# Optimization experiments

Measured on AMD Instinct MI355X. Metric: run time of the kernel, lower is better.

## Reference

```python
import jax, jax.numpy as jnp
import numpy as np

H = 384
W = 384
C_X = 64       # channels of x (== out_channels)
C_PTX = 64     # channels of ptx
C_IN = C_X + C_PTX  # Linear in_channels = 128
C_OUT = 64
N_TGT = 120000  # number of target pixels (CSR segments)
DEG = 8         # points per target pixel
N_PTS = N_TGT * DEG


def setup_inputs() -> dict:
    key = jax.random.key(0)
    k1, k2, k3, k4 = jax.random.split(key, 4)
    x = jax.random.normal(k1, (1, C_X, H, W), jnp.float32)
    ptx = jax.random.normal(k2, (N_PTS, C_PTX), jnp.float32)
    # CSR row pointer over points per target pixel (monotone, ends at N_PTS)
    point_key = jnp.arange(N_TGT + 1, dtype=jnp.int32) * DEG
    # unique target-pixel indices into H*W
    pixel_tgt_idx = jnp.arange(N_TGT, dtype=jnp.int32)
    sm_w = jax.random.normal(k3, (C_IN, 1), jnp.float32) * 0.05
    sm_b = jnp.zeros((1,), jnp.float32)
    fo_w = jax.random.normal(k4, (C_IN, C_OUT), jnp.float32) * 0.05
    fo_b = jnp.zeros((C_OUT,), jnp.float32)
    return {"x": x, "ptx": ptx, "sm_w": sm_w, "sm_b": sm_b,
            "fo_w": fo_w, "fo_b": fo_b, "point_key": point_key,
            "pixel_tgt_idx": pixel_tgt_idx, "bs": 1, "height": H, "width": W}


def reference(x, ptx, sm_w, sm_b, fo_w, fo_b, point_key, pixel_tgt_idx, bs, height, width):
    # segment id per point from CSR rowptr (static total length for jit)
    seg = jnp.repeat(jnp.arange(N_TGT, dtype=jnp.int32), jnp.diff(point_key),
                     total_repeat_length=N_PTS)
    # pixel features gathered to target pixels, then CSR-gathered to points
    feat_px = x.transpose(0, 2, 3, 1).reshape(height * width, C_X)[pixel_tgt_idx]
    feat = jnp.concatenate([ptx, feat_px[seg]], axis=1)  # [N_PTS, C_IN]
    # _net_forward: identity (base class)
    # segment softmax over points within each pixel group
    logits = feat @ sm_w + sm_b  # [N_PTS, 1]
    m = jax.ops.segment_max(logits, seg, num_segments=N_TGT)
    e = jnp.exp(logits - m[seg])
    s = jax.ops.segment_sum(e, seg, num_segments=N_TGT)
    weight = e / (s[seg] + 1e-16)
    # feat_out projection replaces ptx
    ptx_out = feat @ fo_w + fo_b  # [N_PTS, C_OUT]
    agg = jax.ops.segment_sum(weight * ptx_out, seg, num_segments=N_TGT)  # [N_TGT, C_OUT]
    # list_to_map: scatter aggregated features back to image grid + mask
    flat = jnp.zeros((height * width, C_OUT), x.dtype).at[pixel_tgt_idx].set(agg)
    mask = jnp.zeros((height * width, 1), x.dtype).at[pixel_tgt_idx].set(1.0)
    fmap = flat.reshape(1, height, width, C_OUT).transpose(0, 3, 1, 2)
    mmap = mask.reshape(1, height, width, 1).transpose(0, 3, 1, 2)
    x_out = jnp.where(mmap > 0, fmap, x)
    return x_out, ptx_out
```

## Files before the change

kernel.cpp:

```cpp
#include <hip/hip_runtime.h>
#include <hip/hip_bf16.h>
#include <math.h>

typedef __attribute__((ext_vector_type(8))) short short8v;
typedef __attribute__((ext_vector_type(4))) float float4v;

__device__ __forceinline__ short f2bf(float f) {
    __hip_bfloat16 h = __float2bfloat16(f);
    short s;
    __builtin_memcpy(&s, &h, sizeof(short));
    return s;
}

__device__ __forceinline__ float4v mfma_bf16(short8v a, short8v b, float4v c) {
    return __builtin_amdgcn_mfma_f32_16x16x32_bf16(a, b, c, 0, 0, 0);
}

__global__ __launch_bounds__(256)
void copy_x_kernel(const float4* __restrict__ x, float4* __restrict__ out, int n4) {
    int i = blockIdx.x * blockDim.x + threadIdx.x;
    if (i < n4) out[i] = x[i];
}

__global__ __launch_bounds__(256, 3)
void fused_kernel(const float* __restrict__ x,
                  const float* __restrict__ ptx,
                  const float* __restrict__ sm_w,
                  const float* __restrict__ fo_w,
                  const float* __restrict__ fo_b,
                  const int* __restrict__ point_key,
                  const int* __restrict__ pixel_tgt_idx,
                  float* __restrict__ xout,
                  float* __restrict__ ptx_out,
                  int n_tgt, int n_pts, int hw)
{
    __shared__ unsigned short fpx[32][72];
    __shared__ float q_lds[32][68];
    __shared__ float agg_lds[32][68];
    __shared__ int pix_s[32], r0_s[32], deg_s[32];

    const int tid  = threadIdx.x;
    const int lane = tid & 63;
    const int w    = tid >> 6;
    const int t0   = blockIdx.x * 32;
    const int lo16 = lane & 15;
    const int g    = lane >> 4;

    if (tid < 32) {
        int t = t0 + tid;
        bool v = t < n_tgt;
        int r0 = v ? point_key[t] : 0;
        int d  = v ? (point_key[t + 1] - r0) : 0;
        pix_s[tid] = v ? pixel_tgt_idx[t] : 0;
        r0_s[tid]  = r0;
        deg_s[tid] = d > 8 ? 8 : d;
    }
    __syncthreads();

    {
        int tgt = tid & 31, cq = tid >> 5;
        int pix = pix_s[tgt];
        #pragma unroll
        for (int i = 0; i < 8; ++i) {
            int c = cq * 8 + i;
            fpx[tgt][c] = (unsigned short)f2bf(x[(size_t)c * hw + pix]);
        }
    }
    __syncthreads();

    {
        const int mt_q = w & 1;
        const int ctb  = (w >> 1) * 2;
        short8v b2[2][2];
        #pragma unroll
        for (int ci = 0; ci < 2; ++ci)
            #pragma unroll
            for (int kh = 0; kh < 2; ++kh) {
                short8v bb;
                int col = (ctb + ci) * 16 + lo16;
                int kbase = kh * 32 + g * 8;
                #pragma unroll
                for (int j = 0; j < 8; ++j)
                    bb[j] = f2bf(fo_w[(size_t)(64 + kbase + j) * 64 + col]);
                b2[ci][kh] = bb;
            }
        short8v a2[2];
        #pragma unroll
        for (int kh = 0; kh < 2; ++kh) {
            int row = mt_q * 16 + lo16;
            a2[kh] = *(const short8v*)&fpx[row][kh * 32 + g * 8];
        }
        float4v qc0 = {0.f, 0.f, 0.f, 0.f}, qc1 = {0.f, 0.f, 0.f, 0.f};
        qc0 = mfma_bf16(a2[0], b2[0][0], qc0);
        qc0 = mfma_bf16(a2[1], b2[0][1], qc0);
        qc1 = mfma_bf16(a2[0], b2[1][0], qc1);
        qc1 = mfma_bf16(a2[1], b2[1][1], qc1);
        #pragma unroll
        for (int ci = 0; ci < 2; ++ci) {
            int col = (ctb + ci) * 16 + lo16;
            float fb = fo_b[col];
            const float4v& qc = ci ? qc1 : qc0;
            #pragma unroll
            for (int r = 0; r < 4; ++r)
                q_lds[mt_q * 16 + g * 4 + r][col] = qc[r] + fb;
        }
    }

    short8v b1[5][2];
    #pragma unroll
    for (int ct = 0; ct < 5; ++ct)
        #pragma unroll
        for (int kh = 0; kh < 2; ++kh) {
            short8v bb;
            int kbase = kh * 32 + g * 8;
            #pragma unroll
            for (int j = 0; j < 8; ++j) {
                int k = kbase + j;
                float f = (ct < 4) ? fo_w[(size_t)k * 64 + ct * 16 + lo16]
                                   : ((lo16 == 0) ? sm_w[k] : 0.0f);
                bb[j] = f2bf(f);
            }
            b1[ct][kh] = bb;
        }
    __syncthreads();

    const int tw0 = w * 8;
    #pragma unroll
    for (int mt = 0; mt < 4; ++mt) {
        int s_row = mt * 16 + lo16;
        int tlA   = tw0 + (s_row >> 3);
        int pg    = r0_s[tlA] + (s_row & 7);
        if (pg >= n_pts) pg = n_pts - 1;
        const float* prow = ptx + (size_t)pg * 64 + g * 8;
        short8v a[2];
        #pragma unroll
        for (int kh = 0; kh < 2; ++kh) {
            float4 f0 = *(const float4*)(prow + kh * 32);
            float4 f1 = *(const float4*)(prow + kh * 32 + 4);
            short8v aa;
            aa[0] = f2bf(f0.x); aa[1] = f2bf(f0.y); aa[2] = f2bf(f0.z); aa[3] = f2bf(f0.w);
            aa[4] = f2bf(f1.x); aa[5] = f2bf(f1.y); aa[6] = f2bf(f1.z); aa[7] = f2bf(f1.w);
            a[kh] = aa;
        }
        float4v c[5];
        #pragma unroll
        for (int ct = 0; ct < 5; ++ct) {
            float4v z = {0.f, 0.f, 0.f, 0.f};
            z = mfma_bf16(a[0], b1[ct][0], z);
            c[ct] = mfma_bf16(a[1], b1[ct][1], z);
        }

        const int tE   = tw0 + mt * 2 + (g >> 1);
        const int degE = deg_s[tE];
        const int r0E  = r0_s[tE];
        float lgt[4];
        #pragma unroll
        for (int r = 0; r < 4; ++r) {
            float v = __shfl(c[4][r], lane & 48);
            lgt[r] = (((g & 1) * 4 + r) < degE) ? v : -3.4e38f;
        }
        float m4 = fmaxf(fmaxf(lgt[0], lgt[1]), fmaxf(lgt[2], lgt[3]));
        float m8 = fmaxf(m4, __shfl_xor(m4, 16));
        float wgt[4], wsum = 0.f;
        #pragma unroll
        for (int r = 0; r < 4; ++r) {
            int pE = (g & 1) * 4 + r;
            wgt[r] = (pE < degE) ? __expf(lgt[r] - m8) : 0.0f;
            wsum += wgt[r];
        }
        wsum += __shfl_xor(wsum, 16);
        float inv = 1.0f / (wsum + 1e-16f);

        #pragma unroll
        for (int ct = 0; ct < 4; ++ct) {
            int col = ct * 16 + lo16;
            float qv = q_lds[tE][col];
            float ap = 0.f;
            #pragma unroll
            for (int r = 0; r < 4; ++r) {
                float po = c[ct][r] + qv;
                int pE = (g & 1) * 4 + r;
                if (pE < degE)
                    ptx_out[(size_t)(r0E + pE) * 64 + col] = po;
                ap = fmaf(wgt[r] * inv, po, ap);
            }
            ap += __shfl_xor(ap, 16);
            if (!(lane & 16))
                agg_lds[tE][col] = ap;
        }
    }
    __syncthreads();

    {
        int tgt = tid & 31, cq = tid >> 5;
        if (t0 + tgt < n_tgt) {
            int pix = pix_s[tgt];
            #pragma unroll
            for (int i = 0; i < 8; ++i) {
                int c = cq * 8 + i;
                xout[(size_t)c * hw + pix] = agg_lds[tgt][c];
            }
        }
    }
}

extern "C" void kernel_launch(void* const* d_in, const int* in_sizes, int n_in,
                              void* d_out, int out_size, void* d_ws, size_t ws_size,
                              hipStream_t stream) {
    const float* x             = (const float*)d_in[0];
    const float* ptx           = (const float*)d_in[1];
    const float* sm_w          = (const float*)d_in[2];
    const float* fo_w          = (const float*)d_in[4];
    const float* fo_b          = (const float*)d_in[5];
    const int*   point_key     = (const int*)d_in[6];
    const int*   pixel_tgt_idx = (const int*)d_in[7];

    const int x_elems = in_sizes[0];
    const int hw      = x_elems / 64;
    const int n_tgt   = in_sizes[7];
    const int n_pts   = in_sizes[1] / 64;

    float* xout    = (float*)d_out;
    float* ptx_out = xout + (size_t)x_elems;

    const int n4 = x_elems / 4;
    copy_x_kernel<<<(n4 + 255) / 256, 256, 0, stream>>>(
        (const float4*)x, (float4*)xout, n4);

    const int blocks = (n_tgt + 31) / 32;
    fused_kernel<<<blocks, 256, 0, stream>>>(
        x, ptx, sm_w, fo_w, fo_b, point_key, pixel_tgt_idx,
        xout, ptx_out, n_tgt, n_pts, hw);
}
```

Before: 141.4 us.

## Process 128 targets per block with LDS-staged transposed weights and register q

Each block now handles 128 targets instead of 32, so the per-block cost of loading and converting fo_w is spread over four times as many points. The weights are staged once through LDS with coalesced float4 reads and stored transposed in bf16. The per-pixel projection q is kept in registers and distributed with shuffles instead of going through an LDS table, and the agg buffer reuses the same shared memory. The trade-off is fewer blocks (about 938), a longer per-block serial loop and higher register pressure, which could reduce latency hiding.

```diff
diff --git a/kernel.cpp b/kernel.cpp
--- a/kernel.cpp
+++ b/kernel.cpp
@@ -5,13 +5,13 @@
 typedef __attribute__((ext_vector_type(8))) short short8v;
 typedef __attribute__((ext_vector_type(4))) float float4v;
 
+#define TB 128
+
 __device__ __forceinline__ short f2bf(float f) {
     __hip_bfloat16 h = __float2bfloat16(f);
-    short s;
-    __builtin_memcpy(&s, &h, sizeof(short));
+    short s; __builtin_memcpy(&s, &h, sizeof(short));
     return s;
 }
-
 __device__ __forceinline__ float4v mfma_bf16(short8v a, short8v b, float4v c) {
     return __builtin_amdgcn_mfma_f32_16x16x32_bf16(a, b, c, 0, 0, 0);
 }
@@ -34,19 +34,20 @@
                   float* __restrict__ ptx_out,
                   int n_tgt, int n_pts, int hw)
 {
-    __shared__ unsigned short fpx[32][72];
-    __shared__ float q_lds[32][68];
-    __shared__ float agg_lds[32][68];
-    __shared__ int pix_s[32], r0_s[32], deg_s[32];
+    __shared__ __align__(16) char sraw[2 * 128 * 72 * 2];
+    unsigned short (*fpx)[72] = (unsigned short (*)[72])sraw;
+    unsigned short (*wT)[72]  = (unsigned short (*)[72])(sraw + 128 * 72 * 2);
+    float (*agg)[68]          = (float (*)[68])sraw;
+    __shared__ int pix_s[TB], r0_s[TB], deg_s[TB];
 
     const int tid  = threadIdx.x;
     const int lane = tid & 63;
     const int w    = tid >> 6;
-    const int t0   = blockIdx.x * 32;
     const int lo16 = lane & 15;
     const int g    = lane >> 4;
-
-    if (tid < 32) {
+    const int t0   = blockIdx.x * TB;
+
+    if (tid < TB) {
         int t = t0 + tid;
         bool v = t < n_tgt;
         int r0 = v ? point_key[t] : 0;
@@ -55,150 +56,165 @@
         r0_s[tid]  = r0;
         deg_s[tid] = d > 8 ? 8 : d;
     }
-    __syncthreads();
-
-    {
-        int tgt = tid & 31, cq = tid >> 5;
-        int pix = pix_s[tgt];
+    {
+        const float4* fw4 = (const float4*)fo_w;
         #pragma unroll
         for (int i = 0; i < 8; ++i) {
-            int c = cq * 8 + i;
-            fpx[tgt][c] = (unsigned short)f2bf(x[(size_t)c * hw + pix]);
-        }
-    }
-    __syncthreads();
-
-    {
-        const int mt_q = w & 1;
-        const int ctb  = (w >> 1) * 2;
-        short8v b2[2][2];
-        #pragma unroll
-        for (int ci = 0; ci < 2; ++ci)
+            int idx4 = i * 256 + tid;
+            float4 v = fw4[idx4];
+            int flat = idx4 * 4;
+            int k = flat >> 6, c = flat & 63;
+            int wrow0 = (k & 64) + c;
+            int col = k & 63;
+            wT[wrow0 + 0][col] = (unsigned short)f2bf(v.x);
+            wT[wrow0 + 1][col] = (unsigned short)f2bf(v.y);
+            wT[wrow0 + 2][col] = (unsigned short)f2bf(v.z);
+            wT[wrow0 + 3][col] = (unsigned short)f2bf(v.w);
+        }
+    }
+    __syncthreads();
+
+    {
+        const int tgt = tid >> 1, half = tid & 1;
+        const int pix = pix_s[tgt];
+        const float* xp = x + (size_t)(half * 32) * hw + pix;
+        #pragma unroll
+        for (int ch = 0; ch < 4; ++ch) {
+            short8v pk;
+            #pragma unroll
+            for (int j = 0; j < 8; ++j)
+                pk[j] = f2bf(xp[(size_t)(ch * 8 + j) * hw]);
+            *(short8v*)&fpx[tgt][half * 32 + ch * 8] = pk;
+        }
+    }
+    short8v b1[5][2];
+    #pragma unroll
+    for (int ct = 0; ct < 4; ++ct)
+        #pragma unroll
+        for (int kh = 0; kh < 2; ++kh)
+            b1[ct][kh] = *(const short8v*)&wT[ct * 16 + lo16][kh * 32 + g * 8];
+    #pragma unroll
+    for (int kh = 0; kh < 2; ++kh) {
+        short8v bb;
+        #pragma unroll
+        for (int j = 0; j < 8; ++j)
+            bb[j] = (lo16 == 0) ? f2bf(sm_w[kh * 32 + g * 8 + j]) : (short)0;
+        b1[4][kh] = bb;
+    }
+    float fb[4];
+    #pragma unroll
+    for (int ct = 0; ct < 4; ++ct) fb[ct] = fo_b[ct * 16 + lo16];
+    __syncthreads();
+
+    const int tw0 = w * 32;
+    float4v qreg[2][4];
+    {
+        short8v a2[2][2];
+        #pragma unroll
+        for (int mq = 0; mq < 2; ++mq)
+            #pragma unroll
+            for (int kh = 0; kh < 2; ++kh)
+                a2[mq][kh] = *(const short8v*)&fpx[tw0 + mq * 16 + lo16][kh * 32 + g * 8];
+        #pragma unroll
+        for (int ct = 0; ct < 4; ++ct) {
+            short8v b20 = *(const short8v*)&wT[64 + ct * 16 + lo16][g * 8];
+            short8v b21 = *(const short8v*)&wT[64 + ct * 16 + lo16][32 + g * 8];
+            #pragma unroll
+            for (int mq = 0; mq < 2; ++mq) {
+                float4v z = {0.f, 0.f, 0.f, 0.f};
+                z = mfma_bf16(a2[mq][0], b20, z);
+                z = mfma_bf16(a2[mq][1], b21, z);
+                #pragma unroll
+                for (int r = 0; r < 4; ++r) qreg[mq][ct][r] = z[r] + fb[ct];
+            }
+        }
+    }
+    __syncthreads();
+
+    #pragma unroll
+    for (int mq = 0; mq < 2; ++mq)
+    for (int mtl2 = 0; mtl2 < 4; ++mtl2) {
+        #pragma unroll
+        for (int u = 0; u < 2; ++u) {
+            const int mt  = mq * 8 + mtl2 * 2 + u;
+            const int tlA = tw0 + mt * 2 + (lo16 >> 3);
+            int pg = r0_s[tlA] + (lo16 & 7);
+            if (pg >= n_pts) pg = n_pts - 1;
+            const float* prow = ptx + (size_t)pg * 64 + g * 8;
+            short8v a[2];
             #pragma unroll
             for (int kh = 0; kh < 2; ++kh) {
-                short8v bb;
-                int col = (ctb + ci) * 16 + lo16;
-                int kbase = kh * 32 + g * 8;
+                float4 f0 = *(const float4*)(prow + kh * 32);
+                float4 f1 = *(const float4*)(prow + kh * 32 + 4);
+                short8v aa;
+                aa[0] = f2bf(f0.x); aa[1] = f2bf(f0.y); aa[2] = f2bf(f0.z); aa[3] = f2bf(f0.w);
+                aa[4] = f2bf(f1.x); aa[5] = f2bf(f1.y); aa[6] = f2bf(f1.z); aa[7] = f2bf(f1.w);
+                a[kh] = aa;
+            }
+            float4v c[5];
+            #pragma unroll
+            for (int ct = 0; ct < 5; ++ct) {
+                float4v z = {0.f, 0.f, 0.f, 0.f};
+                z = mfma_bf16(a[0], b1[ct][0], z);
+                c[ct] = mfma_bf16(a[1], b1[ct][1], z);
+            }
+
+            const int tE   = tw0 + mt * 2 + (g >> 1);
+            const int degE = deg_s[tE];
+            const int r0E  = r0_s[tE];
+            float lgt[4];
+            #pragma unroll
+            for (int r = 0; r < 4; ++r) {
+                float v = __shfl(c[4][r], lane & 48);
+                lgt[r] = (((g & 1) * 4 + r) < degE) ? v : -3.4e38f;
+            }
+            float m4 = fmaxf(fmaxf(lgt[0], lgt[1]), fmaxf(lgt[2], lgt[3]));
+            float m8 = fmaxf(m4, __shfl_xor(m4, 16));
+            float wgt[4], wsum = 0.f;
+            #pragma unroll
+            for (int r = 0; r < 4; ++r) {
+                int pE = (g & 1) * 4 + r;
+                wgt[r] = (pE < degE) ? __expf(lgt[r] - m8) : 0.0f;
+                wsum += wgt[r];
+            }
+            wsum += __shfl_xor(wsum, 16);
+            const float inv = 1.0f / (wsum + 1e-16f);
+
+            const int srcLane = mtl2 * 16 + lo16;
+            #pragma unroll
+            for (int ct = 0; ct < 4; ++ct) {
+                float q0 = __shfl(qreg[mq][ct][2 * u],     srcLane);
+                float q1 = __shfl(qreg[mq][ct][2 * u + 1], srcLane);
+                float qv = (g & 2) ? q1 : q0;
+                int col = ct * 16 + lo16;
+                float ap = 0.f;
                 #pragma unroll
-                for (int j = 0; j < 8; ++j)
-                    bb[j] = f2bf(fo_w[(size_t)(64 + kbase + j) * 64 + col]);
-                b2[ci][kh] = bb;
-            }
-        short8v a2[2];
-        #pragma unroll
-        for (int kh = 0; kh < 2; ++kh) {
-            int row = mt_q * 16 + lo16;
-            a2[kh] = *(const short8v*)&fpx[row][kh * 32 + g * 8];
-        }
-        float4v qc0 = {0.f, 0.f, 0.f, 0.f}, qc1 = {0.f, 0.f, 0.f, 0.f};
-        qc0 = mfma_bf16(a2[0], b2[0][0], qc0);
-        qc0 = mfma_bf16(a2[1], b2[0][1], qc0);
-        qc1 = mfma_bf16(a2[0], b2[1][0], qc1);
-        qc1 = mfma_bf16(a2[1], b2[1][1], qc1);
-        #pragma unroll
-        for (int ci = 0; ci < 2; ++ci) {
-            int col = (ctb + ci) * 16 + lo16;
-            float fb = fo_b[col];
-            const float4v& qc = ci ? qc1 : qc0;
-            #pragma unroll
-            for (int r = 0; r < 4; ++r)
-                q_lds[mt_q * 16 + g * 4 + r][col] = qc[r] + fb;
-        }
-    }
-
-    short8v b1[5][2];
-    #pragma unroll
-    for (int ct = 0; ct < 5; ++ct)
-        #pragma unroll
-        for (int kh = 0; kh < 2; ++kh) {
-            short8v bb;
-            int kbase = kh * 32 + g * 8;
-            #pragma unroll
-            for (int j = 0; j < 8; ++j) {
-                int k = kbase + j;
-                float f = (ct < 4) ? fo_w[(size_t)k * 64 + ct * 16 + lo16]
-                                   : ((lo16 == 0) ? sm_w[k] : 0.0f);
-                bb[j] = f2bf(f);
-            }
-            b1[ct][kh] = bb;
-        }
-    __syncthreads();
-
-    const int tw0 = w * 8;
-    #pragma unroll
-    for (int mt = 0; mt < 4; ++mt) {
-        int s_row = mt * 16 + lo16;
-        int tlA   = tw0 + (s_row >> 3);
-        int pg    = r0_s[tlA] + (s_row & 7);
-        if (pg >= n_pts) pg = n_pts - 1;
-        const float* prow = ptx + (size_t)pg * 64 + g * 8;
-        short8v a[2];
-        #pragma unroll
-        for (int kh = 0; kh < 2; ++kh) {
-            float4 f0 = *(const float4*)(prow + kh * 32);
-            float4 f1 = *(const float4*)(prow + kh * 32 + 4);
-            short8v aa;
-            aa[0] = f2bf(f0.x); aa[1] = f2bf(f0.y); aa[2] = f2bf(f0.z); aa[3] = f2bf(f0.w);
-            aa[4] = f2bf(f1.x); aa[5] = f2bf(f1.y); aa[6] = f2bf(f1.z); aa[7] = f2bf(f1.w);
-            a[kh] = aa;
-        }
-        float4v c[5];
-        #pragma unroll
-        for (int ct = 0; ct < 5; ++ct) {
-            float4v z = {0.f, 0.f, 0.f, 0.f};
-            z = mfma_bf16(a[0], b1[ct][0], z);
-            c[ct] = mfma_bf16(a[1], b1[ct][1], z);
-        }
-
-        const int tE   = tw0 + mt * 2 + (g >> 1);
-        const int degE = deg_s[tE];
-        const int r0E  = r0_s[tE];
-        float lgt[4];
-        #pragma unroll
-        for (int r = 0; r < 4; ++r) {
-            float v = __shfl(c[4][r], lane & 48);
-            lgt[r] = (((g & 1) * 4 + r) < degE) ? v : -3.4e38f;
-        }
-        float m4 = fmaxf(fmaxf(lgt[0], lgt[1]), fmaxf(lgt[2], lgt[3]));
-        float m8 = fmaxf(m4, __shfl_xor(m4, 16));
-        float wgt[4], wsum = 0.f;
-        #pragma unroll
-        for (int r = 0; r < 4; ++r) {
-            int pE = (g & 1) * 4 + r;
-            wgt[r] = (pE < degE) ? __expf(lgt[r] - m8) : 0.0f;
-            wsum += wgt[r];
-        }
-        wsum += __shfl_xor(wsum, 16);
-        float inv = 1.0f / (wsum + 1e-16f);
-
-        #pragma unroll
-        for (int ct = 0; ct < 4; ++ct) {
-            int col = ct * 16 + lo16;
-            float qv = q_lds[tE][col];
-            float ap = 0.f;
-            #pragma unroll
-            for (int r = 0; r < 4; ++r) {
-                float po = c[ct][r] + qv;
-                int pE = (g & 1) * 4 + r;
-                if (pE < degE)
-                    ptx_out[(size_t)(r0E + pE) * 64 + col] = po;
-                ap = fmaf(wgt[r] * inv, po, ap);
-            }
-            ap += __shfl_xor(ap, 16);
-            if (!(lane & 16))
-                agg_lds[tE][col] = ap;
-        }
-    }
-    __syncthreads();
-
-    {
-        int tgt = tid & 31, cq = tid >> 5;
+                for (int r = 0; r < 4; ++r) {
+                    float po = c[ct][r] + qv;
+                    int pE = (g & 1) * 4 + r;
+                    if (pE < degE)
+                        ptx_out[(size_t)(r0E + pE) * 64 + col] = po;
+                    ap = fmaf(wgt[r] * inv, po, ap);
+                }
+                ap += __shfl_xor(ap, 16);
+                if (!(lane & 16)) agg[tE][col] = ap;
+            }
+        }
+    }
+    __syncthreads();
+
+    {
+        const int tgt = tid >> 1, half = tid & 1;
         if (t0 + tgt < n_tgt) {
-            int pix = pix_s[tgt];
-            #pragma unroll
-            for (int i = 0; i < 8; ++i) {
-                int c = cq * 8 + i;
-                xout[(size_t)c * hw + pix] = agg_lds[tgt][c];
+            const int pix = pix_s[tgt];
+            float* xp = xout + (size_t)(half * 32) * hw + pix;
+            #pragma unroll
+            for (int ch = 0; ch < 8; ++ch) {
+                float4 v = *(const float4*)&agg[tgt][half * 32 + ch * 4];
+                xp[(size_t)(ch * 4 + 0) * hw] = v.x;
+                xp[(size_t)(ch * 4 + 1) * hw] = v.y;
+                xp[(size_t)(ch * 4 + 2) * hw] = v.z;
+                xp[(size_t)(ch * 4 + 3) * hw] = v.w;
             }
         }
     }
@@ -227,7 +243,7 @@
     copy_x_kernel<<<(n4 + 255) / 256, 256, 0, stream>>>(
         (const float4*)x, (float4*)xout, n4);
 
-    const int blocks = (n_tgt + 31) / 32;
+    const int blocks = (n_tgt + TB - 1) / TB;
     fused_kernel<<<blocks, 256, 0, stream>>>(
         x, ptx, sm_w, fo_w, fo_b, point_key, pixel_tgt_idx,
         xout, ptx_out, n_tgt, n_pts, hw);
```

After: 155.1 us. 9.7% more time.
